# Optimization experiments

Hardware: AMD Instinct MI355X
Metric: run time of the kernel (lower is better)

## Reference

```python
import jax, jax.numpy as jnp
import numpy as np

SEQ_LEN = 2048


def setup_inputs() -> dict:
    key = jax.random.key(0)
    k1, k2 = jax.random.split(key)
    x = jax.random.normal(k1, (2, 16, SEQ_LEN, SEQ_LEN), dtype=jnp.float32)
    # nn.Linear(seq_len, seq_len) with kaiming_normal_(fan_in, relu): std = sqrt(2/fan_in)
    W = jax.random.normal(k2, (SEQ_LEN, SEQ_LEN), dtype=jnp.float32) * np.sqrt(2.0 / SEQ_LEN)
    b = jnp.zeros((SEQ_LEN,), dtype=jnp.float32)
    return {"x": x, "W": W, "b": b}


def reference(x, W, b):
    # Original: idx = first argmax of softmax(x, -1); softmax is monotonic so
    # argmax over the raw logits gives the identical (first-occurrence) index
    # without materializing the [B,H,S,S] softmax.
    idx = jnp.argmax(x, axis=-1)                                   # [B,H,S] int
    gathered = jnp.take_along_axis(x, idx[..., None], axis=-1)[..., 0]  # [B,H,S]
    # Linear(seq_len->seq_len) over the seq axis, then exact (erf) GELU as in torch default
    y = jax.nn.gelu(jnp.einsum('bhs,ts->bht', gathered, W) + b, approximate=False)  # [B,H,S]
    # Scatter the transformed values back into x at the argmax positions
    B, H, S, _ = x.shape
    bi = jnp.arange(B)[:, None, None]
    hi = jnp.arange(H)[None, :, None]
    si = jnp.arange(S)[None, None, :]
    return x.at[bi, hi, si, idx].set(y)
```

## Files before the change

### kernel.cpp

```cpp
#include <hip/hip_runtime.h>
#include <math.h>

constexpr int S      = 2048;
constexpr int BH     = 32;
constexpr int NROWS  = BH * S;
constexpr int KS     = 16;
constexpr int KR     = S / KS;

typedef float v4f __attribute__((ext_vector_type(4)));


__global__ __launch_bounds__(256) void rowmax_copy_kernel(
    const float* __restrict__ x, float* __restrict__ out,
    float* __restrict__ G, int* __restrict__ IDX)
{
    const int wave = threadIdx.x >> 6;
    const int lane = threadIdx.x & 63;
    const int row  = blockIdx.x * 4 + wave;

    const v4f* xr   = (const v4f*)(x   + (size_t)row * S);
    v4f*       outr = (v4f*)      (out + (size_t)row * S);

    v4f v[8];
    #pragma unroll
    for (int c = 0; c < 8; ++c)
        v[c] = __builtin_nontemporal_load(xr + c * 64 + lane);

    #pragma unroll
    for (int c = 0; c < 8; ++c)
        __builtin_nontemporal_store(v[c], outr + c * 64 + lane);

    float best = -INFINITY;
    int   bidx = 0;
    #pragma unroll
    for (int c = 0; c < 8; ++c) {
        const int base = (c * 64 + lane) * 4;
        if (v[c].x > best) { best = v[c].x; bidx = base;     }
        if (v[c].y > best) { best = v[c].y; bidx = base + 1; }
        if (v[c].z > best) { best = v[c].z; bidx = base + 2; }
        if (v[c].w > best) { best = v[c].w; bidx = base + 3; }
    }
    #pragma unroll
    for (int off = 32; off > 0; off >>= 1) {
        float ov = __shfl_down(best, off, 64);
        int   oi = __shfl_down(bidx, off, 64);
        if (ov > best || (ov == best && oi < bidx)) { best = ov; bidx = oi; }
    }
    if (lane == 0) {
        G[row]   = best;
        IDX[row] = bidx;
    }
}

__global__ __launch_bounds__(256) void gemm_part_kernel(
    const float* __restrict__ G, const float* __restrict__ W,
    float* __restrict__ part)
{
    const int tid = threadIdx.x;
    const int t   = blockIdx.x * 128 + (tid & 127);
    const int bhb = (tid >> 7) * 16;
    const int k0  = blockIdx.y * KR;

    float acc[16];
    #pragma unroll
    for (int i = 0; i < 16; ++i) acc[i] = 0.0f;

    const v4f*   wr = (const v4f*)(W + (size_t)t * S + k0);
    const float* gp = G + bhb * S + k0;

    #pragma unroll 2
    for (int k = 0; k < KR; k += 4) {
        const v4f w = wr[k >> 2];
        #pragma unroll
        for (int i = 0; i < 16; ++i) {
            const float* g = gp + i * S + k;
            acc[i] += w.x * g[0] + w.y * g[1] + w.z * g[2] + w.w * g[3];
        }
    }

    #pragma unroll
    for (int i = 0; i < 16; ++i) {
        part[(size_t)(blockIdx.y * BH + bhb + i) * S + t] = acc[i];
    }
}

__global__ __launch_bounds__(256) void finish_kernel(
    const float* __restrict__ part, const float* __restrict__ bias,
    const int* __restrict__ IDX, float* __restrict__ out)
{
    const int o  = blockIdx.x * 256 + threadIdx.x;
    const int t  = o & (S - 1);
    const int bh = o >> 11;

    float s = bias[t];
    #pragma unroll
    for (int ks = 0; ks < KS; ++ks)
        s += part[(size_t)(ks * BH + bh) * S + t];

    const float y = 0.5f * s * (1.0f + erff(s * 0.70710678118654752440f));

    const int idx = IDX[o];
    out[(size_t)o * S + idx] = y;
}

extern "C" void kernel_launch(void* const* d_in, const int* in_sizes, int n_in,
                              void* d_out, int out_size, void* d_ws, size_t ws_size,
                              hipStream_t stream) {
    const float* x = (const float*)d_in[0];
    const float* W = (const float*)d_in[1];
    const float* b = (const float*)d_in[2];
    float* out = (float*)d_out;

    float* G    = (float*)d_ws;
    int*   IDX  = (int*)  ((char*)d_ws + (size_t)NROWS * 4);
    float* part = (float*)((char*)d_ws + (size_t)2 * NROWS * 4);

    rowmax_copy_kernel<<<NROWS / 4, 256, 0, stream>>>(x, out, G, IDX);

    dim3 gridB(S / 128, KS);
    gemm_part_kernel<<<gridB, 256, 0, stream>>>(G, W, part);

    finish_kernel<<<NROWS / 256, 256, 0, stream>>>(part, b, IDX, out);
}
```

Measured before the change: 868.2 us.

## Fuse GEMV, GELU and scatter into one kernel with LDS-staged G

Replaces the split-K partial GEMM plus finish kernel with a single kernel that stages 16 rows of gathered maxima in shared memory. Each wave computes dot products for two output columns via lane-parallel K reduction and shuffles, then applies bias, erf-GELU and scatters into the output. This removes the partial-sum buffer round trip and one launch, and converts uncoalesced global G reads into LDS reads. In exchange it uses 128 KiB of LDS per block and only 256 blocks, limiting occupancy.

```diff
diff --git a/kernel.cpp b/kernel.cpp
--- a/kernel.cpp
+++ b/kernel.cpp
@@ -4,8 +4,6 @@
 constexpr int S      = 2048;
 constexpr int BH     = 32;
 constexpr int NROWS  = BH * S;
-constexpr int KS     = 16;
-constexpr int KR     = S / KS;
 
 typedef float v4f __attribute__((ext_vector_type(4)));
 
@@ -52,55 +50,76 @@
     }
 }
 
-__global__ __launch_bounds__(256) void gemm_part_kernel(
+__global__ __launch_bounds__(512) void gemm_gelu_scatter_kernel(
     const float* __restrict__ G, const float* __restrict__ W,
-    float* __restrict__ part)
+    const float* __restrict__ bias, const int* __restrict__ IDX,
+    float* __restrict__ out)
 {
-    const int tid = threadIdx.x;
-    const int t   = blockIdx.x * 128 + (tid & 127);
-    const int bhb = (tid >> 7) * 16;
-    const int k0  = blockIdx.y * KR;
+    __shared__ float g_lds[16 * S];
+    const int tid  = threadIdx.x;
+    const int lane = tid & 63;
+    const int wv   = tid >> 6;
+    const int bh0  = blockIdx.y * 16;
+    const int t0   = blockIdx.x * 16;
 
-    float acc[16];
+    {
+        const v4f* gsrc = (const v4f*)(G + (size_t)bh0 * S);
+        v4f* gdst = (v4f*)g_lds;
+        #pragma unroll
+        for (int r = 0; r < 16; ++r)
+            gdst[tid + r * 512] = gsrc[tid + r * 512];
+    }
+    __syncthreads();
+
+    const int tA = t0 + wv;
+    const int tB = t0 + 8 + wv;
+
+    float accA[16], accB[16];
     #pragma unroll
-    for (int i = 0; i < 16; ++i) acc[i] = 0.0f;
+    for (int i = 0; i < 16; ++i) { accA[i] = 0.0f; accB[i] = 0.0f; }
 
-    const v4f*   wr = (const v4f*)(W + (size_t)t * S + k0);
-    const float* gp = G + bhb * S + k0;
+    const v4f* wrA = (const v4f*)(W + (size_t)tA * S);
+    const v4f* wrB = (const v4f*)(W + (size_t)tB * S);
 
-    #pragma unroll 2
-    for (int k = 0; k < KR; k += 4) {
-        const v4f w = wr[k >> 2];
+    #pragma unroll
+    for (int c = 0; c < 8; ++c) {
+        const int kv = c * 64 + lane;
+        const v4f wa = wrA[kv];
+        const v4f wb = wrB[kv];
         #pragma unroll
         for (int i = 0; i < 16; ++i) {
-            const float* g = gp + i * S + k;
-            acc[i] += w.x * g[0] + w.y * g[1] + w.z * g[2] + w.w * g[3];
+            const v4f g = *(const v4f*)&g_lds[i * S + kv * 4];
+            accA[i] += wa.x * g.x + wa.y * g.y + wa.z * g.z + wa.w * g.w;
+            accB[i] += wb.x * g.x + wb.y * g.y + wb.z * g.z + wb.w * g.w;
         }
     }
 
     #pragma unroll
     for (int i = 0; i < 16; ++i) {
-        part[(size_t)(blockIdx.y * BH + bhb + i) * S + t] = acc[i];
+        #pragma unroll
+        for (int off = 32; off > 0; off >>= 1) {
+            accA[i] += __shfl_xor(accA[i], off, 64);
+            accB[i] += __shfl_xor(accB[i], off, 64);
+        }
     }
-}
 
-__global__ __launch_bounds__(256) void finish_kernel(
-    const float* __restrict__ part, const float* __restrict__ bias,
-    const int* __restrict__ IDX, float* __restrict__ out)
-{
-    const int o  = blockIdx.x * 256 + threadIdx.x;
-    const int t  = o & (S - 1);
-    const int bh = o >> 11;
+    float yA = accA[0], yB = accB[0];
+    #pragma unroll
+    for (int i = 1; i < 16; ++i) {
+        if (lane == i) { yA = accA[i]; yB = accB[i]; }
+    }
 
-    float s = bias[t];
-    #pragma unroll
-    for (int ks = 0; ks < KS; ++ks)
-        s += part[(size_t)(ks * BH + bh) * S + t];
-
-    const float y = 0.5f * s * (1.0f + erff(s * 0.70710678118654752440f));
-
-    const int idx = IDX[o];
-    out[(size_t)o * S + idx] = y;
+    if (lane < 16) {
+        const int bh = bh0 + lane;
+        float sA = yA + bias[tA];
+        float sB = yB + bias[tB];
+        sA = 0.5f * sA * (1.0f + erff(sA * 0.70710678118654752440f));
+        sB = 0.5f * sB * (1.0f + erff(sB * 0.70710678118654752440f));
+        const size_t rA = (size_t)bh * S + tA;
+        const size_t rB = (size_t)bh * S + tB;
+        out[rA * S + IDX[rA]] = sA;
+        out[rB * S + IDX[rB]] = sB;
+    }
 }
 
 extern "C" void kernel_launch(void* const* d_in, const int* in_sizes, int n_in,
@@ -111,14 +130,11 @@
     const float* b = (const float*)d_in[2];
     float* out = (float*)d_out;
 
-    float* G    = (float*)d_ws;
-    int*   IDX  = (int*)  ((char*)d_ws + (size_t)NROWS * 4);
-    float* part = (float*)((char*)d_ws + (size_t)2 * NROWS * 4);
+    float* G   = (float*)d_ws;
+    int*   IDX = (int*)  ((char*)d_ws + (size_t)NROWS * 4);
 
     rowmax_copy_kernel<<<NROWS / 4, 256, 0, stream>>>(x, out, G, IDX);
 
-    dim3 gridB(S / 128, KS);
-    gemm_part_kernel<<<gridB, 256, 0, stream>>>(G, W, part);
-
-    finish_kernel<<<NROWS / 256, 256, 0, stream>>>(part, b, IDX, out);
+    dim3 gridBC(S / 16, 2);
+    gemm_gelu_scatter_kernel<<<gridBC, 512, 0, stream>>>(G, W, b, IDX, out);
 }
```

Result: faster. 847.7 us (-2.4%).
